# Kernel tuning notes

Measured on AMD Instinct MI355X. Metric: run time of the kernel, lower is better.

The kernel has to match this reference:

```python
import jax, jax.numpy as jnp
import numpy as np

N, C, E = 4096, 128, 10          # nodes, channels, element types
LMAX = 2
NI = (LMAX + 1) ** 2             # 9 spherical components of node_feats
K = {1: 4, 2: 12, 3: 30}         # number of CG paths per correlation order
DIMS = [2 * L + 1 for L in range(LMAX + 1)]  # output irrep dims [1,3,5]


def setup_inputs() -> dict:
    key = jax.random.key(0)
    ks = iter(jax.random.split(key, 64))
    inp = {}
    inp["node_feats"] = jax.random.normal(next(ks), (N, C, NI), jnp.float32)
    inp["sc"] = jax.random.normal(next(ks), (N, C * sum(DIMS)), jnp.float32)
    z = jax.random.randint(next(ks), (N,), 0, E)
    inp["node_attrs"] = jax.nn.one_hot(z, E, dtype=jnp.float32)
    for L, d in enumerate(DIMS):
        # U tensors: fixed Clebsch-Gordan-structured constants (stand-in values,
        # correct shapes/contraction pattern of MACE's U_matrix buffers).
        inp[f"U3_L{L}"] = jax.random.normal(next(ks), (d, NI, NI, NI, K[3]), jnp.float32) * 0.05
        inp[f"U2_L{L}"] = jax.random.normal(next(ks), (d, NI, NI, K[2]), jnp.float32) * 0.05
        inp[f"U1_L{L}"] = jax.random.normal(next(ks), (d, NI, K[1]), jnp.float32) * 0.05
        # Element-dependent path weights [num_elements, k, channels]
        inp[f"W3_L{L}"] = jax.random.normal(next(ks), (E, K[3], C), jnp.float32) / np.sqrt(K[3])
        inp[f"W2_L{L}"] = jax.random.normal(next(ks), (E, K[2], C), jnp.float32) / np.sqrt(K[2])
        inp[f"W1_L{L}"] = jax.random.normal(next(ks), (E, K[1], C), jnp.float32) / np.sqrt(K[1])
        # o3.Linear channel-mixing weight for this irrep
        inp[f"lin_L{L}"] = jax.random.normal(next(ks), (C, C), jnp.float32)
    return inp


def _contract(x, y, U3, U2, U1, W3, W2, W1):
    """MACE symmetric contraction (correlation=3) for one output irrep.
    x: [b,c,n] node feats, y: [b,e] one-hot element attrs.
    Recursive einsum structure from mace.modules.symmetric_contraction.Contraction."""
    out = jnp.einsum('dijnk,ekc,bcn,be->bcdij', U3, W3, x, y)
    c2 = jnp.einsum('dijk,ekc,be->bcdij', U2, W2, y) + out
    out = jnp.einsum('bcdij,bcj->bcdi', c2, x)
    c1 = jnp.einsum('dik,ekc,be->bcdi', U1, W1, y) + out
    return jnp.einsum('bcdi,bci->bcd', c1, x)  # [b,c,d]


def reference(node_feats, sc, node_attrs,
              U3_L0, U2_L0, U1_L0, W3_L0, W2_L0, W1_L0, lin_L0,
              U3_L1, U2_L1, U1_L1, W3_L1, W2_L1, W1_L1, lin_L1,
              U3_L2, U2_L2, U1_L2, W3_L2, W2_L2, W1_L2, lin_L2):
    Us = [(U3_L0, U2_L0, U1_L0), (U3_L1, U2_L1, U1_L1), (U3_L2, U2_L2, U1_L2)]
    Ws = [(W3_L0, W2_L0, W1_L0), (W3_L1, W2_L1, W1_L1), (W3_L2, W2_L2, W1_L2)]
    lins = [lin_L0, lin_L1, lin_L2]
    c = node_feats.shape[1]
    norm = jnp.asarray(1.0 / np.sqrt(c), node_feats.dtype)
    outs = []
    for (u3, u2, u1), (w3, w2, w1), lw in zip(Us, Ws, lins):
        o = _contract(node_feats, node_attrs, u3, u2, u1, w3, w2, w1)  # [b,c,d]
        o = jnp.einsum('bcd,cf->bfd', o, lw) * norm                    # o3.Linear mix
        outs.append(o.reshape(o.shape[0], -1))
    return jnp.concatenate(outs, axis=-1) + sc
```

## Files before the change

### kernel.cpp

```cpp
#include <hip/hip_runtime.h>

#define NNODES 4096
#define NCH    128
#define NE     10
#define PADN   4736
#define NCHUNK 74
#define TSTRIDE 2048
#define DGSTRIDE 672


struct MTab { unsigned short v[220]; };
static constexpr MTab make_mtab() {
    MTab t{};
    int m = 0;
    for (int i = 0; i < 9; ++i) {
        t.v[m++] = (unsigned short)((1 << 12) | (i << 8) | (i << 4) | i);
        for (int j = i; j < 9; ++j) {
            t.v[m++] = (unsigned short)((2 << 12) | (i << 8) | (j << 4) | j);
            for (int n = j; n < 9; ++n)
                t.v[m++] = (unsigned short)((3 << 12) | (i << 8) | (j << 4) | n);
        }
    }
    return t;
}
__constant__ MTab c_mtab = make_mtab();

__global__ __launch_bounds__(1024) void k_prep(
    const float* __restrict__ attrs,
    const float* __restrict__ U3_0, const float* __restrict__ U3_1, const float* __restrict__ U3_2,
    const float* __restrict__ W3_0, const float* __restrict__ W3_1, const float* __restrict__ W3_2,
    const float* __restrict__ U2_0, const float* __restrict__ U2_1, const float* __restrict__ U2_2,
    const float* __restrict__ W2_0, const float* __restrict__ W2_1, const float* __restrict__ W2_2,
    const float* __restrict__ U1_0, const float* __restrict__ U1_1, const float* __restrict__ U1_2,
    const float* __restrict__ W1_0, const float* __restrict__ W1_1, const float* __restrict__ W1_2,
    int* __restrict__ list, int* __restrict__ chunkinfo,
    float* __restrict__ wcat, float* __restrict__ Usym)
{
    int bid = blockIdx.x, t = threadIdx.x;
    if (bid == 0) {
        __shared__ int hist[NE], cur[NE], base[NE + 1], cbase[NE + 1];
        if (t < NE) { hist[t] = 0; cur[t] = 0; }
        __syncthreads();
        int mye[4];
#pragma unroll
        for (int k = 0; k < 4; ++k) {
            int b = k * 1024 + t;
            const float* y = attrs + (size_t)b * NE;
            int e = 0;
#pragma unroll
            for (int u = 0; u < NE; ++u) if (y[u] > 0.5f) e = u;
            mye[k] = e;
            atomicAdd(&hist[e], 1);
        }
        for (int i = t; i < PADN; i += 1024) list[i] = -1;
        __syncthreads();
        if (t == 0) {
            int off = 0, goff = 0;
            for (int e = 0; e < NE; ++e) {
                base[e] = off; cbase[e] = goff;
                int nc = (hist[e] + 63) >> 6;
                off += nc * 64; goff += nc;
            }
            base[NE] = off; cbase[NE] = goff;
        }
        __syncthreads();
        if (t < 80) {
            int info = -1;
            if (t < cbase[NE]) {
                int e = 0;
                while (!(t >= cbase[e] && t < cbase[e + 1])) ++e;
                int k = t - cbase[e];
                int valid = hist[e] - k * 64; if (valid > 64) valid = 64;
                info = (base[e] + k * 64) | (valid << 16) | (e << 24);
            }
            chunkinfo[t] = info;
        }
#pragma unroll
        for (int k = 0; k < 4; ++k) {
            int e = mye[k];
            int pos = atomicAdd(&cur[e], 1);
            list[base[e] + pos] = k * 1024 + t;
        }
    } else if (bid <= 10) {
        int e = bid - 1;
#pragma unroll 1
        for (int L = 0; L < 3; ++L) {
            const float* W1 = (L == 0) ? W1_0 : (L == 1) ? W1_1 : W1_2;
            const float* W2 = (L == 0) ? W2_0 : (L == 1) ? W2_1 : W2_2;
            const float* W3 = (L == 0) ? W3_0 : (L == 1) ? W3_1 : W3_2;
            for (int it = t; it < 48 * 128; it += 1024) {
                int c = it & 127, k = it >> 7;
                float v = 0.0f;
                if (k < 4)       v = W1[((size_t)e * 4 + k) * 128 + c];
                else if (k < 16) v = W2[((size_t)e * 12 + (k - 4)) * 128 + c];
                else if (k < 46) v = W3[((size_t)e * 30 + (k - 16)) * 128 + c];
                wcat[(((size_t)L * NE + e) * 48 + k) * 128 + c] = v;
            }
        }
    } else {
        int D = bid - 11;
        const float *U3, *U2, *U1; int dloc;
        if (D == 0)      { U3 = U3_0; U2 = U2_0; U1 = U1_0; dloc = 0; }
        else if (D < 4)  { U3 = U3_1; U2 = U2_1; U1 = U1_1; dloc = D - 1; }
        else             { U3 = U3_2; U2 = U2_2; U1 = U1_2; dloc = D - 4; }
        for (int it = t; it < 219 * 48; it += 1024) {
            int m = it / 48, k = it - m * 48;
            unsigned mv = c_mtab.v[m];
            int kind = mv >> 12, i = (mv >> 8) & 15, j = (mv >> 4) & 15, n = mv & 15;
            float v = 0.0f;
            if (kind == 1) {
                if (k < 4) v = U1[(size_t)(dloc * 9 + i) * 4 + k];
            } else if (kind == 2) {
                if (k >= 4 && k < 16) {
                    int kk = k - 4;
                    v = U2[(size_t)(dloc * 81 + i * 9 + j) * 12 + kk];
                    if (i != j) v += U2[(size_t)(dloc * 81 + j * 9 + i) * 12 + kk];
                }
            } else {
                if (k >= 16 && k < 46) {
                    int kk = k - 16;
                    v = U3[((size_t)dloc * 729 + i * 81 + j * 9 + n) * 30 + kk];
                    if (i == j) {
                        if (j != n)
                            v += U3[((size_t)dloc * 729 + i * 81 + n * 9 + i) * 30 + kk]
                               + U3[((size_t)dloc * 729 + n * 81 + i * 9 + i) * 30 + kk];
                    } else if (j == n) {
                        v += U3[((size_t)dloc * 729 + j * 81 + i * 9 + j) * 30 + kk]
                           + U3[((size_t)dloc * 729 + j * 81 + j * 9 + i) * 30 + kk];
                    } else {
                        v += U3[((size_t)dloc * 729 + i * 81 + n * 9 + j) * 30 + kk]
                           + U3[((size_t)dloc * 729 + j * 81 + i * 9 + n) * 30 + kk]
                           + U3[((size_t)dloc * 729 + j * 81 + n * 9 + i) * 30 + kk]
                           + U3[((size_t)dloc * 729 + n * 81 + i * 9 + j) * 30 + kk]
                           + U3[((size_t)dloc * 729 + n * 81 + j * 9 + i) * 30 + kk];
                    }
                }
            }
            Usym[((size_t)D * 219 + m) * 48 + k] = v;
        }
    }
}

__global__ __launch_bounds__(256) void k_tab(
    const float* __restrict__ wcat, const float* __restrict__ Usym,
    float* __restrict__ Sws)
{
    int bid = blockIdx.x;
    int e = bid / 12, r = bid - e * 12;
    int dg = r >> 2, mq = r & 3;
    int t = threadIdx.x;
    int c = t & 127;
    int sub = __builtin_amdgcn_readfirstlane(t >> 7);
    int D0 = dg * 3;
    int LA = (D0 == 0) ? 0 : (D0 < 4 ? 1 : 2);
    int LB = (D0 + 1 < 4) ? 1 : 2;

    float wcA[48], wcB[48];
#pragma unroll
    for (int k = 0; k < 48; ++k) {
        wcA[k] = wcat[(((size_t)LA * NE + e) * 48 + k) * 128 + c];
        wcB[k] = wcat[(((size_t)LB * NE + e) * 48 + k) * 128 + c];
    }

    float* outp = Sws + ((size_t)e * NCH + c) * TSTRIDE + dg * DGSTRIDE;
    int m1 = mq * 55 + 55; if (m1 > 219) m1 = 219;
#pragma unroll 1
    for (int m = mq * 55 + sub; m < m1; m += 2) {
        unsigned mv = c_mtab.v[m];
        int kind = mv >> 12;
        const float* up0 = Usym + ((size_t)D0 * 219 + m) * 48;
        const float* up1 = up0 + 219 * 48;
        const float* up2 = up1 + 219 * 48;
        float a0 = 0.0f, a1 = 0.0f, a2 = 0.0f;
        if (kind == 1) {
#pragma unroll
            for (int k = 0; k < 4; ++k) {
                a0 = fmaf(up0[k], wcA[k], a0);
                a1 = fmaf(up1[k], wcB[k], a1);
                a2 = fmaf(up2[k], wcB[k], a2);
            }
        } else if (kind == 2) {
#pragma unroll
            for (int k = 4; k < 16; ++k) {
                a0 = fmaf(up0[k], wcA[k], a0);
                a1 = fmaf(up1[k], wcB[k], a1);
                a2 = fmaf(up2[k], wcB[k], a2);
            }
        } else {
#pragma unroll
            for (int k = 16; k < 46; ++k) {
                a0 = fmaf(up0[k], wcA[k], a0);
                a1 = fmaf(up1[k], wcB[k], a1);
                a2 = fmaf(up2[k], wcB[k], a2);
            }
        }
        outp[m * 3 + 0] = a0;
        outp[m * 3 + 1] = a1;
        outp[m * 3 + 2] = a2;
    }
}

__global__ __launch_bounds__(256) void k_main(
    const float* __restrict__ nf, const int* __restrict__ list,
    const int* __restrict__ chunkinfo, const float* __restrict__ Sws,
    float* __restrict__ pre)
{
    __shared__ __align__(16) float tabs[4][TSTRIDE];
    int c = blockIdx.x;
    int w = threadIdx.x >> 6, lane = threadIdx.x & 63;
    int g = blockIdx.y * 4 + w;
    int info = __builtin_amdgcn_readfirstlane(chunkinfo[g]);
    if (info == -1) return;
    int beg = info & 0xffff;
    int e = (info >> 24) & 0xff;
    int pos = beg + lane;
    int b = list[pos];

    float x[9];
    {
        const float* xp = nf + ((size_t)(b < 0 ? 0 : b) * 128 + c) * 9;
#pragma unroll
        for (int n = 0; n < 9; ++n) x[n] = (b >= 0) ? xp[n] : 0.0f;
    }

    {
        const float4* src = (const float4*)(Sws + ((size_t)e * NCH + c) * TSTRIDE);
        float4* dst = (float4*)tabs[w];
#pragma unroll
        for (int k = 0; k < 8; ++k)
            dst[lane + k * 64] = src[lane + k * 64];
    }

    float* prep = pre + (size_t)c * 9 * PADN;

#pragma unroll 1
    for (int dg = 0; dg < 3; ++dg) {
        const float* s = tabs[w] + dg * DGSTRIDE;
        float a3[3] = {0.0f, 0.0f, 0.0f};
        int p = 0;
#pragma unroll
        for (int i = 0; i < 9; ++i) {
            float a2[3];
#pragma unroll
            for (int d = 0; d < 3; ++d) a2[d] = s[p + d];
            p += 3;
#pragma unroll
            for (int j = i; j < 9; ++j) {
                float a1[3];
#pragma unroll
                for (int d = 0; d < 3; ++d) a1[d] = s[p + d];
                p += 3;
#pragma unroll
                for (int n = j; n < 9; ++n) {
#pragma unroll
                    for (int d = 0; d < 3; ++d) a1[d] = fmaf(s[p + d], x[n], a1[d]);
                    p += 3;
                }
#pragma unroll
                for (int d = 0; d < 3; ++d) a2[d] = fmaf(a1[d], x[j], a2[d]);
            }
#pragma unroll
            for (int d = 0; d < 3; ++d) a3[d] = fmaf(a2[d], x[i], a3[d]);
        }
#pragma unroll
        for (int d = 0; d < 3; ++d)
            prep[(size_t)(dg * 3 + d) * PADN + pos] = a3[d];
    }
}

__global__ __launch_bounds__(256) void k_mix(
    const float* __restrict__ pre, const int* __restrict__ chunkinfo,
    const float* __restrict__ lin0, const float* __restrict__ lin1,
    const float* __restrict__ lin2, float* __restrict__ mixed)
{
    __shared__ __align__(16) float pt[128 * 64];
    int bid = blockIdx.x;
    int nt = bid >> 1;
    int fbase = (bid & 1) * 64;
    int n0 = nt * 64;
    int D = nt / NCHUNK;
    int g = nt - D * NCHUNK;
    if (chunkinfo[g] == -1) return;
    const float* lin = (D == 0) ? lin0 : (D < 4 ? lin1 : lin2);
    int t = threadIdx.x;

    {
        int q4 = (t & 15) * 4;
        int cb = t >> 4;
#pragma unroll
        for (int k = 0; k < 8; ++k) {
            int c = cb + k * 16;
            float4 v = *(const float4*)&pre[(size_t)c * 9 * PADN + n0 + q4];
            *(float4*)&pt[c * 64 + q4] = v;
        }
    }
    __syncthreads();

    int tq = t & 63;
    int f0 = fbase + __builtin_amdgcn_readfirstlane(t >> 6) * 16;
    float acc[16];
#pragma unroll
    for (int f = 0; f < 16; ++f) acc[f] = 0.0f;

#pragma unroll 4
    for (int c = 0; c < 128; ++c) {
        float pv = pt[c * 64 + tq];
        const float* lr = lin + c * 128 + f0;
#pragma unroll
        for (int f = 0; f < 16; ++f)
            acc[f] = fmaf(pv, lr[f], acc[f]);
    }

    const float nrm = 0.08838834764831845f;
#pragma unroll
    for (int f = 0; f < 16; ++f)
        mixed[(size_t)(f0 + f) * 9 * PADN + n0 + tq] = acc[f] * nrm;
}

__global__ __launch_bounds__(256) void k_out(
    const float* __restrict__ mixed, const int* __restrict__ list,
    const int* __restrict__ chunkinfo, const float* __restrict__ sc,
    float* __restrict__ out)
{
    __shared__ float tr[64 * 73];
    int fc = blockIdx.x, g = blockIdx.y;
    if (chunkinfo[g] == -1) return;
    int t = threadIdx.x;
    int fbase = fc * 8;
    int tf = t >> 6, tq = t & 63;

#pragma unroll
    for (int k = 0; k < 18; ++k) {
        int row = k * 4 + tf;
        int f = row / 9, D = row - f * 9;
        float v = mixed[((size_t)(fbase + f) * 9 + D) * PADN + g * 64 + tq];
        tr[tq * 73 + row] = v;
    }
    __syncthreads();

#pragma unroll 1
    for (int k = 0; k < 18; ++k) {
        int idx = k * 256 + t;
        int node = idx / 72, col = idx - node * 72;
        int b = list[g * 64 + node];
        if (b < 0) continue;
        int row, gcol;
        if (col < 8)       { row = col * 9;                       gcol = fbase + col; }
        else if (col < 32) { int u = col - 8;  int f = u / 3, dl = u - f * 3;
                             row = f * 9 + 1 + dl;                gcol = 128 + fbase * 3 + u; }
        else               { int u = col - 32; int f = u / 5, dl = u - f * 5;
                             row = f * 9 + 4 + dl;                gcol = 512 + fbase * 5 + u; }
        out[(size_t)b * 1152 + gcol] = tr[node * 73 + row] + sc[(size_t)b * 1152 + gcol];
    }
}

extern "C" void kernel_launch(void* const* d_in, const int* in_sizes, int n_in,
                              void* d_out, int out_size, void* d_ws, size_t ws_size,
                              hipStream_t stream)
{
    const float* nf    = (const float*)d_in[0];
    const float* sc    = (const float*)d_in[1];
    const float* attrs = (const float*)d_in[2];
    const float *U3s[3], *U2s[3], *U1s[3], *W3s[3], *W2s[3], *W1s[3], *lins[3];
    for (int L = 0; L < 3; ++L) {
        const int o = 3 + 7 * L;
        U3s[L]  = (const float*)d_in[o + 0];
        U2s[L]  = (const float*)d_in[o + 1];
        U1s[L]  = (const float*)d_in[o + 2];
        W3s[L]  = (const float*)d_in[o + 3];
        W2s[L]  = (const float*)d_in[o + 4];
        W1s[L]  = (const float*)d_in[o + 5];
        lins[L] = (const float*)d_in[o + 6];
    }

    float* wsf     = (float*)d_ws;
    int* chunkinfo = (int*)d_ws;
    int* list      = chunkinfo + 80;
    float* Sws   = wsf + 4864;
    float* pre   = Sws + (size_t)NE * NCH * TSTRIDE;
    float* mixed = pre + (size_t)NCH * 9 * PADN;
    float* wcat  = mixed + (size_t)NCH * 9 * PADN;
    float* Usym  = wcat + (size_t)3 * NE * 48 * 128;

    k_prep<<<20, 1024, 0, stream>>>(attrs,
                                    U3s[0], U3s[1], U3s[2], W3s[0], W3s[1], W3s[2],
                                    U2s[0], U2s[1], U2s[2], W2s[0], W2s[1], W2s[2],
                                    U1s[0], U1s[1], U1s[2], W1s[0], W1s[1], W1s[2],
                                    list, chunkinfo, wcat, Usym);
    k_tab<<<120, 256, 0, stream>>>(wcat, Usym, Sws);
    k_main<<<dim3(128, 19), 256, 0, stream>>>(nf, list, chunkinfo, Sws, pre);
    k_mix<<<1332, 256, 0, stream>>>(pre, chunkinfo, lins[0], lins[1], lins[2], mixed);
    k_out<<<dim3(16, NCHUNK), 256, 0, stream>>>(mixed, list, chunkinfo, sc, (float*)d_out);
}
```

Measured before the change: 260.1 us.

## Fuse channel mix with output scatter and regroup main kernel by element

The main contraction kernel now launches one block per (channel, element) and loops its four waves over that element's chunks. The block loads the shared table once into LDS and syncs, instead of each wave copying its own table. The separate mix and output kernels are merged into one kernel that computes the linear channel mix in registers for 16 output features and scatters the result with the skip connection added. This removes the intermediate 'mixed' buffer round trip and one launch. In exchange the fused kernel launches fewer blocks, each doing more work per block, which lowers parallelism.

```diff
diff --git a/kernel.cpp b/kernel.cpp
--- a/kernel.cpp
+++ b/kernel.cpp
@@ -74,6 +74,8 @@
                 info = (base[e] + k * 64) | (valid << 16) | (e << 24);
             }
             chunkinfo[t] = info;
+        } else if (t < 91) {
+            chunkinfo[t] = cbase[t - 80];
         }
 #pragma unroll
         for (int k = 0; k < 4; ++k) {
@@ -205,152 +207,161 @@
     const int* __restrict__ chunkinfo, const float* __restrict__ Sws,
     float* __restrict__ pre)
 {
-    __shared__ __align__(16) float tabs[4][TSTRIDE];
-    int c = blockIdx.x;
-    int w = threadIdx.x >> 6, lane = threadIdx.x & 63;
-    int g = blockIdx.y * 4 + w;
-    int info = __builtin_amdgcn_readfirstlane(chunkinfo[g]);
-    if (info == -1) return;
-    int beg = info & 0xffff;
-    int e = (info >> 24) & 0xff;
-    int pos = beg + lane;
-    int b = list[pos];
-
-    float x[9];
-    {
-        const float* xp = nf + ((size_t)(b < 0 ? 0 : b) * 128 + c) * 9;
-#pragma unroll
-        for (int n = 0; n < 9; ++n) x[n] = (b >= 0) ? xp[n] : 0.0f;
-    }
+    __shared__ __align__(16) float tab[TSTRIDE];
+    int c = blockIdx.x, e = blockIdx.y;
+    int t = threadIdx.x;
+    int w = t >> 6, lane = t & 63;
+    int cb0 = chunkinfo[80 + e], cb1 = chunkinfo[81 + e];
+    if (cb0 >= cb1) return;
 
     {
         const float4* src = (const float4*)(Sws + ((size_t)e * NCH + c) * TSTRIDE);
-        float4* dst = (float4*)tabs[w];
-#pragma unroll
-        for (int k = 0; k < 8; ++k)
-            dst[lane + k * 64] = src[lane + k * 64];
-    }
+        float4* dst = (float4*)tab;
+        dst[t] = src[t];
+        dst[t + 256] = src[t + 256];
+    }
+    __syncthreads();
 
     float* prep = pre + (size_t)c * 9 * PADN;
 
 #pragma unroll 1
-    for (int dg = 0; dg < 3; ++dg) {
-        const float* s = tabs[w] + dg * DGSTRIDE;
-        float a3[3] = {0.0f, 0.0f, 0.0f};
-        int p = 0;
-#pragma unroll
-        for (int i = 0; i < 9; ++i) {
-            float a2[3];
-#pragma unroll
-            for (int d = 0; d < 3; ++d) a2[d] = s[p + d];
-            p += 3;
-#pragma unroll
-            for (int j = i; j < 9; ++j) {
-                float a1[3];
-#pragma unroll
-                for (int d = 0; d < 3; ++d) a1[d] = s[p + d];
+    for (int gi = cb0 + w; gi < cb1; gi += 4) {
+        int info = __builtin_amdgcn_readfirstlane(chunkinfo[gi]);
+        int beg = info & 0xffff;
+        int pos = beg + lane;
+        int b = list[pos];
+
+        float x[9];
+        {
+            const float* xp = nf + ((size_t)(b < 0 ? 0 : b) * 128 + c) * 9;
+#pragma unroll
+            for (int n = 0; n < 9; ++n) x[n] = (b >= 0) ? xp[n] : 0.0f;
+        }
+
+#pragma unroll 1
+        for (int dg = 0; dg < 3; ++dg) {
+            const float* s = tab + dg * DGSTRIDE;
+            float a3[3] = {0.0f, 0.0f, 0.0f};
+            int p = 0;
+#pragma unroll
+            for (int i = 0; i < 9; ++i) {
+                float a2[3];
+#pragma unroll
+                for (int d = 0; d < 3; ++d) a2[d] = s[p + d];
                 p += 3;
 #pragma unroll
-                for (int n = j; n < 9; ++n) {
-#pragma unroll
-                    for (int d = 0; d < 3; ++d) a1[d] = fmaf(s[p + d], x[n], a1[d]);
+                for (int j = i; j < 9; ++j) {
+                    float a1[3];
+#pragma unroll
+                    for (int d = 0; d < 3; ++d) a1[d] = s[p + d];
                     p += 3;
+#pragma unroll
+                    for (int n = j; n < 9; ++n) {
+#pragma unroll
+                        for (int d = 0; d < 3; ++d) a1[d] = fmaf(s[p + d], x[n], a1[d]);
+                        p += 3;
+                    }
+#pragma unroll
+                    for (int d = 0; d < 3; ++d) a2[d] = fmaf(a1[d], x[j], a2[d]);
                 }
 #pragma unroll
-                for (int d = 0; d < 3; ++d) a2[d] = fmaf(a1[d], x[j], a2[d]);
-            }
-#pragma unroll
-            for (int d = 0; d < 3; ++d) a3[d] = fmaf(a2[d], x[i], a3[d]);
-        }
-#pragma unroll
-        for (int d = 0; d < 3; ++d)
-            prep[(size_t)(dg * 3 + d) * PADN + pos] = a3[d];
-    }
-}
-
-__global__ __launch_bounds__(256) void k_mix(
-    const float* __restrict__ pre, const int* __restrict__ chunkinfo,
+                for (int d = 0; d < 3; ++d) a3[d] = fmaf(a2[d], x[i], a3[d]);
+            }
+#pragma unroll
+            for (int d = 0; d < 3; ++d)
+                prep[(size_t)(dg * 3 + d) * PADN + pos] = a3[d];
+        }
+    }
+}
+
+__global__ __launch_bounds__(256) void k_fin(
+    const float* __restrict__ pre, const int* __restrict__ list,
+    const int* __restrict__ chunkinfo, const float* __restrict__ sc,
     const float* __restrict__ lin0, const float* __restrict__ lin1,
-    const float* __restrict__ lin2, float* __restrict__ mixed)
+    const float* __restrict__ lin2, float* __restrict__ out)
 {
-    __shared__ __align__(16) float pt[128 * 64];
-    int bid = blockIdx.x;
-    int nt = bid >> 1;
-    int fbase = (bid & 1) * 64;
-    int n0 = nt * 64;
-    int D = nt / NCHUNK;
-    int g = nt - D * NCHUNK;
-    if (chunkinfo[g] == -1) return;
-    const float* lin = (D == 0) ? lin0 : (D < 4 ? lin1 : lin2);
-    int t = threadIdx.x;
-
-    {
-        int q4 = (t & 15) * 4;
-        int cb = t >> 4;
-#pragma unroll
-        for (int k = 0; k < 8; ++k) {
-            int c = cb + k * 16;
-            float4 v = *(const float4*)&pre[(size_t)c * 9 * PADN + n0 + q4];
-            *(float4*)&pt[c * 64 + q4] = v;
-        }
-    }
-    __syncthreads();
-
-    int tq = t & 63;
-    int f0 = fbase + __builtin_amdgcn_readfirstlane(t >> 6) * 16;
-    float acc[16];
-#pragma unroll
-    for (int f = 0; f < 16; ++f) acc[f] = 0.0f;
-
-#pragma unroll 4
-    for (int c = 0; c < 128; ++c) {
-        float pv = pt[c * 64 + tq];
-        const float* lr = lin + c * 128 + f0;
-#pragma unroll
-        for (int f = 0; f < 16; ++f)
-            acc[f] = fmaf(pv, lr[f], acc[f]);
-    }
-
-    const float nrm = 0.08838834764831845f;
-#pragma unroll
-    for (int f = 0; f < 16; ++f)
-        mixed[(size_t)(f0 + f) * 9 * PADN + n0 + tq] = acc[f] * nrm;
-}
-
-__global__ __launch_bounds__(256) void k_out(
-    const float* __restrict__ mixed, const int* __restrict__ list,
-    const int* __restrict__ chunkinfo, const float* __restrict__ sc,
-    float* __restrict__ out)
-{
-    __shared__ float tr[64 * 73];
-    int fc = blockIdx.x, g = blockIdx.y;
+    __shared__ __align__(16) float smem[8 * 9 * 64 + 3 * 128 * 16];
+    float* pt = smem;
+    float* ls = smem + 8 * 9 * 64;
+    int g = blockIdx.x, fq = blockIdx.y;
     if (chunkinfo[g] == -1) return;
     int t = threadIdx.x;
-    int fbase = fc * 8;
-    int tf = t >> 6, tq = t & 63;
-
-#pragma unroll
-    for (int k = 0; k < 18; ++k) {
-        int row = k * 4 + tf;
-        int f = row / 9, D = row - f * 9;
-        float v = mixed[((size_t)(fbase + f) * 9 + D) * PADN + g * 64 + tq];
-        tr[tq * 73 + row] = v;
-    }
+    int tq = t & 63, ft = t >> 6;
+    int fbase = fq * 16;
+
+#pragma unroll
+    for (int k = 0; k < 24; ++k) {
+        int idx = k * 256 + t;
+        int f = idx & 15, cc = (idx >> 4) & 127, L = idx >> 11;
+        const float* lp = (L == 0) ? lin0 : (L == 1) ? lin1 : lin2;
+        ls[idx] = lp[cc * 128 + fbase + f];
+    }
+
+    float acc[4][9];
+#pragma unroll
+    for (int i = 0; i < 4; ++i)
+#pragma unroll
+        for (int d = 0; d < 9; ++d) acc[i][d] = 0.0f;
+
+#pragma unroll 1
+    for (int ch = 0; ch < 16; ++ch) {
+        int cb = ch * 8;
+        __syncthreads();
+#pragma unroll
+        for (int k = 0; k < 18; ++k) {
+            int idx = k * 256 + t;
+            int q = idx & 63, row = idx >> 6;
+            pt[idx] = pre[((size_t)cb * 9 + row) * PADN + g * 64 + q];
+        }
+        __syncthreads();
+#pragma unroll
+        for (int cc = 0; cc < 8; ++cc) {
+            int c = cb + cc;
+            float pv[9];
+#pragma unroll
+            for (int d = 0; d < 9; ++d) pv[d] = pt[(cc * 9 + d) * 64 + tq];
+            float4 l0 = *(const float4*)&ls[(0 * 128 + c) * 16 + ft * 4];
+            float4 l1 = *(const float4*)&ls[(1 * 128 + c) * 16 + ft * 4];
+            float4 l2 = *(const float4*)&ls[(2 * 128 + c) * 16 + ft * 4];
+            float w0[4] = {l0.x, l0.y, l0.z, l0.w};
+            float w1[4] = {l1.x, l1.y, l1.z, l1.w};
+            float w2[4] = {l2.x, l2.y, l2.z, l2.w};
+#pragma unroll
+            for (int i = 0; i < 4; ++i) {
+                acc[i][0] = fmaf(pv[0], w0[i], acc[i][0]);
+#pragma unroll
+                for (int dl = 0; dl < 3; ++dl)
+                    acc[i][1 + dl] = fmaf(pv[1 + dl], w1[i], acc[i][1 + dl]);
+#pragma unroll
+                for (int dl = 0; dl < 5; ++dl)
+                    acc[i][4 + dl] = fmaf(pv[4 + dl], w2[i], acc[i][4 + dl]);
+            }
+        }
+    }
+
+    float* tr = smem;
+    const float nrm = 0.08838834764831845f;
     __syncthreads();
-
-#pragma unroll 1
-    for (int k = 0; k < 18; ++k) {
+#pragma unroll
+    for (int i = 0; i < 4; ++i)
+#pragma unroll
+        for (int d = 0; d < 9; ++d)
+            tr[tq * 145 + (ft * 4 + i) * 9 + d] = acc[i][d] * nrm;
+    __syncthreads();
+
+#pragma unroll 1
+    for (int k = 0; k < 36; ++k) {
         int idx = k * 256 + t;
-        int node = idx / 72, col = idx - node * 72;
+        int node = idx / 144, col = idx - node * 144;
         int b = list[g * 64 + node];
         if (b < 0) continue;
         int row, gcol;
-        if (col < 8)       { row = col * 9;                       gcol = fbase + col; }
-        else if (col < 32) { int u = col - 8;  int f = u / 3, dl = u - f * 3;
-                             row = f * 9 + 1 + dl;                gcol = 128 + fbase * 3 + u; }
-        else               { int u = col - 32; int f = u / 5, dl = u - f * 5;
-                             row = f * 9 + 4 + dl;                gcol = 512 + fbase * 5 + u; }
-        out[(size_t)b * 1152 + gcol] = tr[node * 73 + row] + sc[(size_t)b * 1152 + gcol];
+        if (col < 16)      { row = col * 9;                         gcol = fbase + col; }
+        else if (col < 64) { int u = col - 16; int lf = u / 3, dl = u - lf * 3;
+                             row = lf * 9 + 1 + dl;                 gcol = 128 + fbase * 3 + u; }
+        else               { int u = col - 64; int lf = u / 5, dl = u - lf * 5;
+                             row = lf * 9 + 4 + dl;                 gcol = 512 + fbase * 5 + u; }
+        out[(size_t)b * 1152 + gcol] = tr[node * 145 + row] + sc[(size_t)b * 1152 + gcol];
     }
 }
 
@@ -375,11 +386,10 @@
 
     float* wsf     = (float*)d_ws;
     int* chunkinfo = (int*)d_ws;
-    int* list      = chunkinfo + 80;
+    int* list      = chunkinfo + 96;
     float* Sws   = wsf + 4864;
     float* pre   = Sws + (size_t)NE * NCH * TSTRIDE;
-    float* mixed = pre + (size_t)NCH * 9 * PADN;
-    float* wcat  = mixed + (size_t)NCH * 9 * PADN;
+    float* wcat  = pre + (size_t)NCH * 9 * PADN;
     float* Usym  = wcat + (size_t)3 * NE * 48 * 128;
 
     k_prep<<<20, 1024, 0, stream>>>(attrs,
@@ -388,7 +398,7 @@
                                     U1s[0], U1s[1], U1s[2], W1s[0], W1s[1], W1s[2],
                                     list, chunkinfo, wcat, Usym);
     k_tab<<<120, 256, 0, stream>>>(wcat, Usym, Sws);
-    k_main<<<dim3(128, 19), 256, 0, stream>>>(nf, list, chunkinfo, Sws, pre);
-    k_mix<<<1332, 256, 0, stream>>>(pre, chunkinfo, lins[0], lins[1], lins[2], mixed);
-    k_out<<<dim3(16, NCHUNK), 256, 0, stream>>>(mixed, list, chunkinfo, sc, (float*)d_out);
-}
+    k_main<<<dim3(128, 10), 256, 0, stream>>>(nf, list, chunkinfo, Sws, pre);
+    k_fin<<<dim3(NCHUNK, 8), 256, 0, stream>>>(pre, list, chunkinfo, sc,
+                                               lins[0], lins[1], lins[2], (float*)d_out);
+}
```

Measured after the change: 297.0 us. 1.14x slower.
